# Performance work log

Hardware: AMD Instinct MI355X
Metric: run time of the kernel (lower is better)

The kernel has to match this reference:

```python
import jax, jax.numpy as jnp
import numpy as np

B, N, C_IN, C_OUT, M = 32, 4096, 128, 128, 256


def setup_inputs() -> dict:
    key = jax.random.key(0)
    k1, k2, k3, k4 = jax.random.split(key, 4)
    x = jax.random.normal(k1, (B, N, C_IN), dtype=jnp.float32)
    # Lowest-M eigenvectors of a graph Laplacian are orthonormal columns [N, M];
    # build an equivalent orthonormal basis via QR of a random matrix.
    U, _ = jnp.linalg.qr(jax.random.normal(k2, (N, M), dtype=jnp.float32))
    # complex spectral weights ~ 0.02 * randn (cfloat) split into real/imag parts
    W_real = jax.random.normal(k3, (C_IN, C_OUT, M), dtype=jnp.float32) * 0.02
    W_imag = jax.random.normal(k4, (C_IN, C_OUT, M), dtype=jnp.float32) * 0.02
    return {"x": x, "eigenvectors": U, "W_real": W_real, "W_imag": W_imag}


def reference(x, eigenvectors, W_real, W_imag):
    # Graph Fourier transform: project node features onto spectral modes.
    # x_spec[b, m, c] = sum_n U[n, m] * x[b, n, c]
    x_spec = jnp.einsum('nm,bnc->bmc', eigenvectors, x)  # [B, M, C_in], real
    # Per-mode complex channel mixing, fused into one batched einsum.
    # Original takes .real of (x_spec * W); since x_spec is real,
    # Re(x_spec @ W) = x_spec @ Re(W), so W_imag does not affect the output.
    out_spec_real = jnp.einsum('bmc,com->bmo', x_spec, W_real)  # [B, M, C_out]
    # Inverse graph Fourier transform back to node space.
    return jnp.einsum('nm,bmo->bno', eigenvectors, out_spec_real)  # [B, N, C_out]
```

## Files before the change

### kernel.cpp

```cpp
#include <hip/hip_runtime.h>
#include <hip/hip_bf16.h>

#define BB 32
#define NN 4096
#define CI 128
#define CO 128
#define MM 256
#define KS 8

typedef __hip_bfloat16 bf16;
typedef __attribute__((ext_vector_type(8))) short bf16x8;
typedef __attribute__((ext_vector_type(4))) float f32x4;

__device__ inline void gl_lds16(const void* g, void* l) {
    __builtin_amdgcn_global_load_lds(
        (const __attribute__((address_space(1))) void*)g,
        (__attribute__((address_space(3))) void*)l, 16, 0, 0);
}

__global__ __launch_bounds__(256) void k_cvtU(const float* __restrict__ U,
                                              bf16* __restrict__ Un,
                                              bf16* __restrict__ Ut) {
    const int n0 = blockIdx.x * 64;
    const int m0 = blockIdx.y * 64;
    __shared__ float tile[64][65];
    const int t = threadIdx.x;
    #pragma unroll
    for (int i = 0; i < 16; ++i) {
        int lin = t + i * 256;
        int r = lin >> 6, c = lin & 63;
        float v = U[(n0 + r) * MM + m0 + c];
        tile[r][c] = v;
        Un[(n0 + r) * MM + m0 + c] = __float2bfloat16(v);
    }
    __syncthreads();
    #pragma unroll
    for (int i = 0; i < 16; ++i) {
        int lin = t + i * 256;
        int r = lin >> 6, c = lin & 63;
        Ut[(long)(m0 + r) * NN + n0 + c] = __float2bfloat16(tile[c][r]);
    }
}

__global__ __launch_bounds__(256) void k_trx(const float* __restrict__ x,
                                             bf16* __restrict__ xT) {
    const int c0 = blockIdx.x * 64;
    const int n0 = blockIdx.y * 64;
    const int b  = blockIdx.z;
    __shared__ float tile[64][65];
    const int t = threadIdx.x;
    #pragma unroll
    for (int i = 0; i < 16; ++i) {
        int lin = t + i * 256;
        int r = lin >> 6, c = lin & 63;
        tile[r][c] = x[((long)b * NN + n0 + r) * CI + c0 + c];
    }
    __syncthreads();
    #pragma unroll
    for (int i = 0; i < 16; ++i) {
        int lin = t + i * 256;
        int r = lin >> 6, c = lin & 63;
        xT[((long)b * CI + c0 + r) * NN + n0 + c] = __float2bfloat16(tile[c][r]);
    }
}

__global__ __launch_bounds__(256) void k_gemm1(const bf16* __restrict__ Ut,
                                               const bf16* __restrict__ xT,
                                               bf16* __restrict__ part) {
    const int ks = blockIdx.x;
    const int m0 = blockIdx.y * 128;
    const int b  = blockIdx.z;
    __shared__ __align__(16) bf16 As[128 * 32];
    __shared__ __align__(16) bf16 Bs[128 * 32];
    const int t    = threadIdx.x;
    const int lane = t & 63;
    const int wave = t >> 6;
    const int wm   = wave >> 1, wn = wave & 1;
    const int fr   = lane & 15;
    const int kg   = (lane >> 4) * 8;
    f32x4 acc[4][4] = {};
    const long xbase = (long)b * CI * NN;
    for (int kt = 0; kt < 512 / 32; ++kt) {
        const int k0 = ks * 512 + kt * 32;
        #pragma unroll
        for (int i = 0; i < 2; ++i) {
            int lin = t + i * 256;
            int r = lin >> 2, kk = (lin & 3) * 8;
            gl_lds16(&Ut[(long)(m0 + r) * NN + k0 + kk], &As[lin * 8]);
            gl_lds16(&xT[xbase + (long)r * NN + k0 + kk], &Bs[lin * 8]);
        }
        __syncthreads();
        bf16x8 a[4], bfr[4];
        #pragma unroll
        for (int i = 0; i < 4; ++i)
            a[i] = *(const bf16x8*)&As[(wm * 64 + i * 16 + fr) * 32 + kg];
        #pragma unroll
        for (int j = 0; j < 4; ++j)
            bfr[j] = *(const bf16x8*)&Bs[(wn * 64 + j * 16 + fr) * 32 + kg];
        #pragma unroll
        for (int i = 0; i < 4; ++i)
            #pragma unroll
            for (int j = 0; j < 4; ++j)
                acc[i][j] = __builtin_amdgcn_mfma_f32_16x16x32_bf16(a[i], bfr[j], acc[i][j], 0, 0, 0);
        __syncthreads();
    }
    const int quad = (lane >> 4) * 4;
    const long pbase = ((long)ks * BB + b) * MM * CI;
    #pragma unroll
    for (int i = 0; i < 4; ++i) {
        #pragma unroll
        for (int j = 0; j < 4; ++j) {
            int mg = m0 + wm * 64 + i * 16 + quad;
            int cg = wn * 64 + j * 16 + fr;
            #pragma unroll
            for (int r = 0; r < 4; ++r)
                part[pbase + (long)(mg + r) * CI + cg] = __float2bfloat16(acc[i][j][r]);
        }
    }
}

__global__ __launch_bounds__(256) void k_mix(const bf16* __restrict__ part,
                                             const float* __restrict__ W,
                                             float* __restrict__ os) {
    const int blk = blockIdx.x;
    const int m   = (blk & 7) * 32 + ((blk >> 3) >> 1);
    const int o0  = ((blk >> 3) & 1) * 64;
    __shared__ float Wl[CI][64];
    __shared__ float xl[BB][CI];
    const int t = threadIdx.x;
    for (int idx = t; idx < CI * 64; idx += 256) {
        int c = idx >> 6, o = idx & 63;
        Wl[c][o] = W[((long)c * CO + o0 + o) * MM + m];
    }
    for (int idx = t; idx < BB * CI; idx += 256) {
        int b = idx >> 7, c = idx & 127;
        float s = 0.f;
        #pragma unroll
        for (int ks = 0; ks < KS; ++ks)
            s += __bfloat162float(part[(((long)ks * BB + b) * MM + m) * CI + c]);
        xl[b][c] = s;
    }
    __syncthreads();
    const int o  = t & 63;
    const int bg = (t >> 6) * 8;
    float acc[8] = {};
    for (int c = 0; c < CI; ++c) {
        float w = Wl[c][o];
        #pragma unroll
        for (int bb = 0; bb < 8; ++bb)
            acc[bb] += xl[bg + bb][c] * w;
    }
    #pragma unroll
    for (int bb = 0; bb < 8; ++bb)
        os[((long)(bg + bb) * MM + m) * CO + o0 + o] = acc[bb];
}

__global__ __launch_bounds__(256) void k_tros(const float* __restrict__ os,
                                              bf16* __restrict__ osT) {
    const int o0 = blockIdx.x * 64;
    const int m0 = blockIdx.y * 64;
    const int b  = blockIdx.z;
    __shared__ float tile[64][65];
    const int t = threadIdx.x;
    #pragma unroll
    for (int i = 0; i < 16; ++i) {
        int lin = t + i * 256;
        int r = lin >> 6, c = lin & 63;
        tile[r][c] = os[((long)b * MM + m0 + r) * CO + o0 + c];
    }
    __syncthreads();
    #pragma unroll
    for (int i = 0; i < 16; ++i) {
        int lin = t + i * 256;
        int r = lin >> 6, c = lin & 63;
        osT[((long)b * CO + o0 + r) * MM + m0 + c] = __float2bfloat16(tile[c][r]);
    }
}

__global__ __launch_bounds__(256) void k_gemm3(const bf16* __restrict__ Un,
                                               const bf16* __restrict__ osT,
                                               float* __restrict__ out) {
    const int n0 = blockIdx.x * 128;
    const int b  = blockIdx.y;
    __shared__ __align__(16) bf16 As[128 * 32];
    __shared__ __align__(16) bf16 Bs[128 * 32];
    const int t    = threadIdx.x;
    const int lane = t & 63;
    const int wave = t >> 6;
    const int wm   = wave >> 1, wn = wave & 1;
    const int fr   = lane & 15;
    const int kg   = (lane >> 4) * 8;
    f32x4 acc[4][4] = {};
    const long bbase = (long)b * CO * MM;
    for (int kt = 0; kt < MM / 32; ++kt) {
        const int k0 = kt * 32;
        #pragma unroll
        for (int i = 0; i < 2; ++i) {
            int lin = t + i * 256;
            int r = lin >> 2, kk = (lin & 3) * 8;
            gl_lds16(&Un[(long)(n0 + r) * MM + k0 + kk], &As[lin * 8]);
            gl_lds16(&osT[bbase + (long)r * MM + k0 + kk], &Bs[lin * 8]);
        }
        __syncthreads();
        bf16x8 a[4], bfr[4];
        #pragma unroll
        for (int i = 0; i < 4; ++i)
            a[i] = *(const bf16x8*)&As[(wm * 64 + i * 16 + fr) * 32 + kg];
        #pragma unroll
        for (int j = 0; j < 4; ++j)
            bfr[j] = *(const bf16x8*)&Bs[(wn * 64 + j * 16 + fr) * 32 + kg];
        #pragma unroll
        for (int i = 0; i < 4; ++i)
            #pragma unroll
            for (int j = 0; j < 4; ++j)
                acc[i][j] = __builtin_amdgcn_mfma_f32_16x16x32_bf16(a[i], bfr[j], acc[i][j], 0, 0, 0);
        __syncthreads();
    }
    const int quad = (lane >> 4) * 4;
    #pragma unroll
    for (int i = 0; i < 4; ++i) {
        #pragma unroll
        for (int j = 0; j < 4; ++j) {
            int ng = n0 + wm * 64 + i * 16 + quad;
            int og = wn * 64 + j * 16 + fr;
            #pragma unroll
            for (int r = 0; r < 4; ++r)
                out[((long)b * NN + ng + r) * CO + og] = acc[i][j][r];
        }
    }
}

extern "C" void kernel_launch(void* const* d_in, const int* in_sizes, int n_in,
                              void* d_out, int out_size, void* d_ws, size_t ws_size,
                              hipStream_t stream) {
    const float* x  = (const float*)d_in[0];
    const float* U  = (const float*)d_in[1];
    const float* Wr = (const float*)d_in[2];
    float* out = (float*)d_out;

    char* p = (char*)d_ws;
    bf16* xT   = (bf16*)p;                 p += (size_t)BB * CI * NN * 2;
    bf16* part = (bf16*)p;                 p += (size_t)KS * BB * MM * CI * 2;
    bf16* Ut   = (bf16*)p;                 p += (size_t)MM * NN * 2;
    bf16* Un   = (bf16*)p;                 p += (size_t)NN * MM * 2;
    bf16* osT  = (bf16*)p;                 p += (size_t)BB * CO * MM * 2;
    float* os  = (float*)p;                p += (size_t)BB * MM * CO * 4;

    k_cvtU <<<dim3(NN / 64, MM / 64), 256, 0, stream>>>(U, Un, Ut);
    k_trx  <<<dim3(CI / 64, NN / 64, BB), 256, 0, stream>>>(x, xT);
    k_gemm1<<<dim3(KS, MM / 128, BB), 256, 0, stream>>>(Ut, xT, part);
    k_mix  <<<dim3(512), 256, 0, stream>>>(part, Wr, os);
    k_tros <<<dim3(CO / 64, MM / 64, BB), 256, 0, stream>>>(os, osT);
    k_gemm3<<<dim3(NN / 128, BB), 256, 0, stream>>>(Un, osT, out);
}
```

Measured before the change: 213.4 us.

## Pre-transpose W to bf16 and fuse output transpose into mixing kernel

Adds a kernel that transposes W_real into a per-mode [M][C_in][C_out] bf16 layout, so the mixing kernel can do contiguous vectorized loads instead of strided gathers along M. The mixing kernel now reads partial sums with 16-byte vector loads and writes bf16 directly into the transposed osT layout, which removes the separate os transpose kernel and its fp32 intermediate buffer. The cost is an extra full pass over W each call and strided scalar stores from the mix kernel. W is also rounded to bf16, which lowers precision.

```diff
diff --git a/kernel.cpp b/kernel.cpp
--- a/kernel.cpp
+++ b/kernel.cpp
@@ -61,6 +61,28 @@
         int lin = t + i * 256;
         int r = lin >> 6, c = lin & 63;
         xT[((long)b * CI + c0 + r) * NN + n0 + c] = __float2bfloat16(tile[c][r]);
+    }
+}
+
+__global__ __launch_bounds__(256) void k_wt(const float* __restrict__ W,
+                                            bf16* __restrict__ Wt) {
+    const int m0 = blockIdx.x * 64;
+    const int o0 = blockIdx.y * 64;
+    const int c  = blockIdx.z;
+    __shared__ float tile[64][65];
+    const int t = threadIdx.x;
+    #pragma unroll
+    for (int i = 0; i < 16; ++i) {
+        int lin = t + i * 256;
+        int r = lin >> 6, col = lin & 63;
+        tile[r][col] = W[((long)c * CO + o0 + r) * MM + m0 + col];
+    }
+    __syncthreads();
+    #pragma unroll
+    for (int i = 0; i < 16; ++i) {
+        int lin = t + i * 256;
+        int r = lin >> 6, col = lin & 63;
+        Wt[((long)(m0 + r) * CI + c) * CO + o0 + col] = __float2bfloat16(tile[col][r]);
     }
 }
 
@@ -120,61 +142,51 @@
 }
 
 __global__ __launch_bounds__(256) void k_mix(const bf16* __restrict__ part,
-                                             const float* __restrict__ W,
-                                             float* __restrict__ os) {
+                                             const bf16* __restrict__ Wt,
+                                             bf16* __restrict__ osT) {
     const int blk = blockIdx.x;
-    const int m   = (blk & 7) * 32 + ((blk >> 3) >> 1);
-    const int o0  = ((blk >> 3) & 1) * 64;
+    const int mi  = blk >> 1;
+    const int m   = (mi & 7) * 32 + (mi >> 3);
+    const int o0  = (blk & 1) * 64;
     __shared__ float Wl[CI][64];
-    __shared__ float xl[BB][CI];
-    const int t = threadIdx.x;
-    for (int idx = t; idx < CI * 64; idx += 256) {
-        int c = idx >> 6, o = idx & 63;
-        Wl[c][o] = W[((long)c * CO + o0 + o) * MM + m];
-    }
-    for (int idx = t; idx < BB * CI; idx += 256) {
-        int b = idx >> 7, c = idx & 127;
-        float s = 0.f;
-        #pragma unroll
-        for (int ks = 0; ks < KS; ++ks)
-            s += __bfloat162float(part[(((long)ks * BB + b) * MM + m) * CI + c]);
-        xl[b][c] = s;
-    }
-    __syncthreads();
-    const int o  = t & 63;
-    const int bg = (t >> 6) * 8;
+    __shared__ float xl[CI][36];
+    const int t = threadIdx.x;
+    const long wb = (long)m * CI * CO;
+    #pragma unroll
+    for (int i = 0; i < 4; ++i) {
+        int ch = t + i * 256;
+        int c = ch >> 3, og = (ch & 7) * 8;
+        bf16x8 v = *(const bf16x8*)&Wt[wb + (long)c * CO + o0 + og];
+        #pragma unroll
+        for (int j = 0; j < 8; ++j) Wl[c][og + j] = __bfloat162float(((const bf16*)&v)[j]);
+    }
+    #pragma unroll
+    for (int i = 0; i < 2; ++i) {
+        int ch = t + i * 256;
+        int b = ch >> 4, c8 = (ch & 15) * 8;
+        float s[8] = {};
+        #pragma unroll
+        for (int ks = 0; ks < KS; ++ks) {
+            bf16x8 v = *(const bf16x8*)&part[(((long)ks * BB + b) * MM + m) * CI + c8];
+            #pragma unroll
+            for (int j = 0; j < 8; ++j) s[j] += __bfloat162float(((const bf16*)&v)[j]);
+        }
+        #pragma unroll
+        for (int j = 0; j < 8; ++j) xl[c8 + j][b] = s[j];
+    }
+    __syncthreads();
+    const int op = t & 63;
+    const int bq = t >> 6;
     float acc[8] = {};
     for (int c = 0; c < CI; ++c) {
-        float w = Wl[c][o];
-        #pragma unroll
-        for (int bb = 0; bb < 8; ++bb)
-            acc[bb] += xl[bg + bb][c] * w;
-    }
-    #pragma unroll
-    for (int bb = 0; bb < 8; ++bb)
-        os[((long)(bg + bb) * MM + m) * CO + o0 + o] = acc[bb];
-}
-
-__global__ __launch_bounds__(256) void k_tros(const float* __restrict__ os,
-                                              bf16* __restrict__ osT) {
-    const int o0 = blockIdx.x * 64;
-    const int m0 = blockIdx.y * 64;
-    const int b  = blockIdx.z;
-    __shared__ float tile[64][65];
-    const int t = threadIdx.x;
-    #pragma unroll
-    for (int i = 0; i < 16; ++i) {
-        int lin = t + i * 256;
-        int r = lin >> 6, c = lin & 63;
-        tile[r][c] = os[((long)b * MM + m0 + r) * CO + o0 + c];
-    }
-    __syncthreads();
-    #pragma unroll
-    for (int i = 0; i < 16; ++i) {
-        int lin = t + i * 256;
-        int r = lin >> 6, c = lin & 63;
-        osT[((long)b * CO + o0 + r) * MM + m0 + c] = __float2bfloat16(tile[c][r]);
-    }
+        float w = Wl[c][op];
+        #pragma unroll
+        for (int j = 0; j < 8; ++j)
+            acc[j] += xl[c][bq * 8 + j] * w;
+    }
+    #pragma unroll
+    for (int j = 0; j < 8; ++j)
+        osT[((long)(bq * 8 + j) * CO + o0 + op) * MM + m] = __float2bfloat16(acc[j]);
 }
 
 __global__ __launch_bounds__(256) void k_gemm3(const bf16* __restrict__ Un,
@@ -239,17 +251,17 @@
     float* out = (float*)d_out;
 
     char* p = (char*)d_ws;
-    bf16* xT   = (bf16*)p;                 p += (size_t)BB * CI * NN * 2;
-    bf16* part = (bf16*)p;                 p += (size_t)KS * BB * MM * CI * 2;
-    bf16* Ut   = (bf16*)p;                 p += (size_t)MM * NN * 2;
-    bf16* Un   = (bf16*)p;                 p += (size_t)NN * MM * 2;
-    bf16* osT  = (bf16*)p;                 p += (size_t)BB * CO * MM * 2;
-    float* os  = (float*)p;                p += (size_t)BB * MM * CO * 4;
+    bf16* xT   = (bf16*)p;  p += (size_t)BB * CI * NN * 2;
+    bf16* part = (bf16*)p;  p += (size_t)KS * BB * MM * CI * 2;
+    bf16* Ut   = (bf16*)p;  p += (size_t)MM * NN * 2;
+    bf16* Un   = (bf16*)p;  p += (size_t)NN * MM * 2;
+    bf16* osT  = (bf16*)p;  p += (size_t)BB * CO * MM * 2;
+    bf16* Wt   = (bf16*)p;  p += (size_t)MM * CI * CO * 2;
 
     k_cvtU <<<dim3(NN / 64, MM / 64), 256, 0, stream>>>(U, Un, Ut);
     k_trx  <<<dim3(CI / 64, NN / 64, BB), 256, 0, stream>>>(x, xT);
+    k_wt   <<<dim3(MM / 64, CO / 64, CI), 256, 0, stream>>>(Wr, Wt);
     k_gemm1<<<dim3(KS, MM / 128, BB), 256, 0, stream>>>(Ut, xT, part);
-    k_mix  <<<dim3(512), 256, 0, stream>>>(part, Wr, os);
-    k_tros <<<dim3(CO / 64, MM / 64, BB), 256, 0, stream>>>(os, osT);
+    k_mix  <<<dim3(512), 256, 0, stream>>>(part, Wt, osT);
     k_gemm3<<<dim3(NN / 128, BB), 256, 0, stream>>>(Un, osT, out);
 }
```

Measured after the change: 200.7 us. 1.06x faster.
